# Kernel optimization log

Measured on AMD Instinct MI355X. Metric: run time of the kernel, lower is better.

## Reference

```python
import jax, jax.numpy as jnp
import numpy as np

WIN = 32      # window_size
SHIFT = 16    # shift_size
EPS = 1e-5

def layernorm(x, w, b):
    mu = jnp.mean(x, axis=-1, keepdims=True)
    var = jnp.mean(jnp.square(x - mu), axis=-1, keepdims=True)
    return (x - mu) * jax.lax.rsqrt(var + EPS) * w + b

def setup_inputs() -> dict:
    key = jax.random.key(0)
    ks = jax.random.split(key, 6)
    B, N, C, H = 8, 4096, 512, 2048
    nW = N // WIN
    return {
        "q": jax.random.normal(ks[0], (B, N, C), jnp.float32),
        "kv": jax.random.normal(ks[1], (B, N, C), jnp.float32),
        "attn_mask": jax.random.normal(ks[2], (nW, WIN, WIN), jnp.float32),
        "norm1_w": jnp.ones((C,), jnp.float32),
        "norm1_b": jnp.zeros((C,), jnp.float32),
        "norm2_w": jnp.ones((C,), jnp.float32),
        "norm2_b": jnp.zeros((C,), jnp.float32),
        "fc1_w": jax.random.normal(ks[3], (H, C), jnp.float32) * 0.02,
        "fc1_b": jnp.zeros((H,), jnp.float32),
        "fc2_w": jax.random.normal(ks[4], (C, H), jnp.float32) * 0.02,
        "fc2_b": jnp.zeros((C,), jnp.float32),
    }

def reference(q, kv, attn_mask, norm1_w, norm1_b, norm2_w, norm2_b,
              fc1_w, fc1_b, fc2_w, fc2_b):
    B, N, C = q.shape
    nW = N // WIN
    shortcut = kv
    qn = layernorm(q, norm1_w, norm1_b)
    kn = layernorm(kv, norm1_w, norm1_b)
    # cyclic shift
    qs = jnp.roll(qn, -SHIFT, axis=1)
    ks = jnp.roll(kn, -SHIFT, axis=1)
    qw = qs.reshape(B * nW, WIN, C)
    kw = ks.reshape(B * nW, WIN, C)
    attn = jnp.einsum('bic,bjc->bij', qw, kw)
    attn = attn.reshape(B, nW, WIN, WIN) + attn_mask[None]
    attn = jax.nn.softmax(attn.reshape(B * nW, WIN, WIN), axis=-1)
    x = jnp.einsum('bij,bjc->bic', attn, kw)
    x = jnp.swapaxes(x, 1, 2).reshape(B * nW, WIN, C)
    # window reverse + reverse shift
    x = x.reshape(B, N, C)
    x = jnp.roll(x, SHIFT, axis=1)
    kv_out = shortcut + x
    # MLP (exact erf GELU, dropout identity at eval)
    h = layernorm(kv_out, norm2_w, norm2_b)
    h = jax.nn.gelu(h @ fc1_w.T + fc1_b, approximate=False)
    h = h @ fc2_w.T + fc2_b
    return kv_out + h
```

## Files before the change

### kernel.cpp

```cpp
#include <hip/hip_runtime.h>
#include <cstdint>
#include <cstddef>


typedef __attribute__((ext_vector_type(4)))  float f32x4;
typedef __attribute__((ext_vector_type(16))) float f32x16;
typedef __attribute__((ext_vector_type(8)))  __bf16 bf16x8;
typedef __attribute__((ext_vector_type(8)))  unsigned short us8;
typedef __attribute__((ext_vector_type(4)))  unsigned short us4;

__device__ __forceinline__ unsigned short f2bf(float f) {
  unsigned int u = __builtin_bit_cast(unsigned int, f);
  u += 0x7fffu + ((u >> 16) & 1u);
  return (unsigned short)(u >> 16);
}

#define GLDS16(g, l)                                                         \
  __builtin_amdgcn_global_load_lds(                                          \
      (const __attribute__((address_space(1))) void*)(g),                    \
      (__attribute__((address_space(3))) void*)(l), 16, 0, 0)

__global__ __launch_bounds__(256) void wconv_kernel(
    const float* __restrict__ w1, const float* __restrict__ w2,
    unsigned short* __restrict__ o1, unsigned short* __restrict__ o2) {
  const int i = (blockIdx.x * 256 + threadIdx.x) * 4;
  const f32x4 a = *(const f32x4*)(w1 + i);
  us4 pa; pa[0]=f2bf(a[0]); pa[1]=f2bf(a[1]); pa[2]=f2bf(a[2]); pa[3]=f2bf(a[3]);
  *(us4*)(o1 + i) = pa;
  const f32x4 b = *(const f32x4*)(w2 + i);
  us4 pb; pb[0]=f2bf(b[0]); pb[1]=f2bf(b[1]); pb[2]=f2bf(b[2]); pb[3]=f2bf(b[3]);
  *(us4*)(o2 + i) = pb;
}

__global__ __launch_bounds__(256) void stats_kernel(
    const float* __restrict__ qg, const float* __restrict__ kvg,
    float* __restrict__ stats) {
  const int gw = (blockIdx.x * 256 + threadIdx.x) >> 6;
  const int l  = threadIdx.x & 63;
  const int s  = gw & 1;
  const int row = gw >> 1;
  const float* src = (s ? kvg : qg) + (size_t)row * 512 + l * 8;
  const f32x4 v0 = *(const f32x4*)(src);
  const f32x4 v1 = *(const f32x4*)(src + 4);
  float a = 0.f, a2 = 0.f;
#pragma unroll
  for (int m = 0; m < 4; ++m) {
    a += v0[m] + v1[m];
    a2 += v0[m] * v0[m] + v1[m] * v1[m];
  }
#pragma unroll
  for (int mm = 1; mm <= 32; mm <<= 1) {
    a += __shfl_xor(a, mm); a2 += __shfl_xor(a2, mm);
  }
  if (l == 0) {
    const float mu = a * (1.f / 512.f);
    const float rs = rsqrtf(a2 * (1.f / 512.f) - mu * mu + 1e-5f);
    *(float2*)(stats + (size_t)row * 4 + s * 2) = make_float2(mu, rs);
  }
}

__global__ __launch_bounds__(128) void attn2_kernel(
    const float* __restrict__ qg, const float* __restrict__ kvg,
    const float* __restrict__ maskg,
    const float* __restrict__ n1w, const float* __restrict__ n1b,
    const float* __restrict__ n2w, const float* __restrict__ n2b,
    const float* __restrict__ stats,
    float* __restrict__ kv_out, unsigned short* __restrict__ hn) {
  __shared__ __align__(16) float xch[2][4][64][4];

  const int t  = threadIdx.x;
  const int h  = t >> 6;
  const int l  = t & 63;
  const int il = l & 31;
  const int hi = l >> 5;
  const int g  = blockIdx.x;
  const int b  = g >> 7;
  const int wi = g & 127;
  const int wbase = wi * 32 + 16;

  const int nrow = (wbase + il) & 4095;
  const size_t rowidx = (size_t)b * 4096 + nrow;
  const float* qrow = qg  + rowidx * 512;
  const float* krow = kvg + rowidx * 512;
  const f32x4 st = *(const f32x4*)(stats + rowidx * 4);

  f32x16 sacc = {};
#pragma unroll
  for (int t16 = 0; t16 < 16; ++t16) {
    const int kk = h * 256 + t16 * 16 + hi * 8;
    const f32x4 qa = *(const f32x4*)(qrow + kk);
    const f32x4 qb = *(const f32x4*)(qrow + kk + 4);
    const f32x4 ka = *(const f32x4*)(krow + kk);
    const f32x4 kb = *(const f32x4*)(krow + kk + 4);
    const f32x4 wa = *(const f32x4*)(n1w + kk);
    const f32x4 wb = *(const f32x4*)(n1w + kk + 4);
    const f32x4 ba = *(const f32x4*)(n1b + kk);
    const f32x4 bb = *(const f32x4*)(n1b + kk + 4);
    bf16x8 qh, ql, kh, kl;
#pragma unroll
    for (int e = 0; e < 8; ++e) {
      const float qe = (e < 4) ? qa[e] : qb[e - 4];
      const float ke = (e < 4) ? ka[e] : kb[e - 4];
      const float we = (e < 4) ? wa[e] : wb[e - 4];
      const float be = (e < 4) ? ba[e] : bb[e - 4];
      const float qn = (qe - st[0]) * st[1] * we + be;
      const float kn = (ke - st[2]) * st[3] * we + be;
      const __bf16 qhb = (__bf16)qn;
      const __bf16 khb = (__bf16)kn;
      qh[e] = qhb; ql[e] = (__bf16)(qn - (float)qhb);
      kh[e] = khb; kl[e] = (__bf16)(kn - (float)khb);
    }
    sacc = __builtin_amdgcn_mfma_f32_32x32x16_bf16(kh, qh, sacc, 0, 0, 0);
    sacc = __builtin_amdgcn_mfma_f32_32x32x16_bf16(kh, ql, sacc, 0, 0, 0);
    sacc = __builtin_amdgcn_mfma_f32_32x32x16_bf16(kl, qh, sacc, 0, 0, 0);
  }

#pragma unroll
  for (int qd = 0; qd < 4; ++qd) {
    f32x4 v = {sacc[qd*4+0], sacc[qd*4+1], sacc[qd*4+2], sacc[qd*4+3]};
    *(f32x4*)&xch[h][qd][l][0] = v;
  }
  __syncthreads();
  float sv[16];
#pragma unroll
  for (int qd = 0; qd < 4; ++qd) {
    const f32x4 v = *(const f32x4*)&xch[1 - h][qd][l][0];
#pragma unroll
    for (int m = 0; m < 4; ++m) sv[qd*4+m] = sacc[qd*4+m] + v[m];
  }

  const float* mrow = maskg + (size_t)wi * 1024 + il * 32;
  float mx = -1e30f;
#pragma unroll
  for (int r = 0; r < 16; ++r) {
    const int j = (r & 3) + 8 * (r >> 2) + 4 * hi;
    sv[r] += mrow[j];
    mx = fmaxf(mx, sv[r]);
  }
  mx = fmaxf(mx, __shfl_xor(mx, 32));
  float P[16], sum = 0.f;
#pragma unroll
  for (int r = 0; r < 16; ++r) { P[r] = __expf(sv[r] - mx); sum += P[r]; }
  sum += __shfl_xor(sum, 32);
  const float inv = 1.f / sum;

  const float rs_own = st[3];
  const float ms_own = st[2] * st[3];
  float Pp[16], beta = 0.f;
#pragma unroll
  for (int r = 0; r < 16; ++r) {
    const int j = (r & 3) + 8 * (r >> 2) + 4 * hi;
    const float rsj = __shfl(rs_own, j);
    const float msj = __shfl(ms_own, j);
    P[r] *= inv;
    beta -= P[r] * msj;
    Pp[r] = P[r] * rsj;
  }
  beta += __shfl_xor(beta, 32);
  float breg[16];
#pragma unroll
  for (int r = 0; r < 16; ++r) {
    const int ir = (r & 3) + 8 * (r >> 2) + 4 * hi;
    breg[r] = __shfl(beta, ir);
  }

  float Ps[16];
#pragma unroll
  for (int r = 0; r < 16; ++r) Ps[r] = __shfl_xor(Pp[r], 32);
  bf16x8 pa[2];
#pragma unroll
  for (int s = 0; s < 2; ++s) {
#pragma unroll
    for (int m = 0; m < 8; ++m) {
      float v;
      if (m < 4) v = (hi == 0) ? Pp[8*s+m] : Ps[8*s+m+4];
      else       v = (hi == 1) ? Pp[8*s+m] : Ps[8*s+m-4];
      pa[s][m] = (__bf16)v;
    }
  }

  const size_t bbase = (size_t)b * 4096;
#pragma unroll 2
  for (int nt = 0; nt < 8; ++nt) {
    const int c = h * 256 + nt * 32 + il;
    const float* kvc = kvg + bbase * 512 + c;
    bf16x8 pb0, pb1;
#pragma unroll
    for (int e = 0; e < 8; ++e) {
      const int j0 = 8 * hi + e;
      const int r0 = (wbase + j0) & 4095;
      pb0[e] = (__bf16)kvc[(size_t)r0 * 512];
      const int r1 = (wbase + j0 + 16) & 4095;
      pb1[e] = (__bf16)kvc[(size_t)r1 * 512];
    }
    f32x16 x = {};
    x = __builtin_amdgcn_mfma_f32_32x32x16_bf16(pa[0], pb0, x, 0, 0, 0);
    x = __builtin_amdgcn_mfma_f32_32x32x16_bf16(pa[1], pb1, x, 0, 0, 0);

    const int p  = h * 16 + nt * 2 + (il >> 4);
    const int np = (wbase + p) & 4095;
    const size_t orow = (bbase + np) * 512;
    const float w1c = n1w[c], b1c = n1b[c];
    float ov[16], s1 = 0.f, s2 = 0.f;
#pragma unroll
    for (int qd = 0; qd < 4; ++qd) {
      const int q0 = (il & 15) * 32 + 8 * qd + 4 * hi;
      const f32x4 rv = *(const f32x4*)(kvg + orow + q0);
      f32x4 o;
#pragma unroll
      for (int m = 0; m < 4; ++m) {
        const int r = qd * 4 + m;
        const float xv = w1c * (x[r] + breg[r]) + b1c;
        o[m] = xv + rv[m];
        s1 += o[m]; s2 += o[m] * o[m];
        ov[r] = o[m];
      }
      *(f32x4*)(kv_out + orow + q0) = o;
    }
#pragma unroll
    for (int mm = 1; mm <= 8; mm <<= 1) {
      s1 += __shfl_xor(s1, mm); s2 += __shfl_xor(s2, mm);
    }
    s1 += __shfl_xor(s1, 32); s2 += __shfl_xor(s2, 32);
    const float mu2 = s1 * (1.f / 512.f);
    const float rr  = rsqrtf(s2 * (1.f / 512.f) - mu2 * mu2 + 1e-5f);
#pragma unroll
    for (int qd = 0; qd < 4; ++qd) {
      const int q0 = (il & 15) * 32 + 8 * qd + 4 * hi;
      const f32x4 w2v = *(const f32x4*)(n2w + q0);
      const f32x4 b2v = *(const f32x4*)(n2b + q0);
      us4 hh;
#pragma unroll
      for (int m = 0; m < 4; ++m)
        hh[m] = f2bf((ov[qd*4+m] - mu2) * rr * w2v[m] + b2v[m]);
      *(us4*)(hn + orow + q0) = hh;
    }
  }
}

__global__ __launch_bounds__(256) void gemm1_kernel(
    const unsigned short* __restrict__ A, const unsigned short* __restrict__ Bw,
    const float* __restrict__ bias, unsigned short* __restrict__ Y) {
  __shared__ __align__(16) char smem[32768];

  const int tid = threadIdx.x;
  const int m0 = blockIdx.x << 7;
  const int n0 = blockIdx.y << 7;
  const int l  = tid & 63;
  const int wv = tid >> 6;
  const int wr = wv >> 1, wc = wv & 1;
  const int srow = tid >> 2;
  const int scol = (tid & 3) << 3;
  const int lrow = l & 15;
  const int lko  = (l >> 4) << 3;

  f32x4 acc[4][4] = {};
  const unsigned short* pA = A  + (size_t)(m0 + srow) * 512 + scol;
  const unsigned short* pB = Bw + (size_t)(n0 + srow) * 512 + scol;

#define G1_STAGE(p, kt)                                                      \
  {                                                                          \
    char* base = smem + (p) * 16384;                                         \
    GLDS16(pA + (kt) * 32,            base + wv * 1024);                     \
    GLDS16(pA + 64 * 512 + (kt) * 32, base + 4096 + wv * 1024);              \
    GLDS16(pB + (kt) * 32,            base + 8192 + wv * 1024);              \
    GLDS16(pB + 64 * 512 + (kt) * 32, base + 12288 + wv * 1024);             \
  }

  G1_STAGE(0, 0);
  __syncthreads();
  for (int kt = 0; kt < 16; ++kt) {
    const int p = kt & 1;
    if (kt < 15) G1_STAGE(p ^ 1, kt + 1);
    const unsigned short* As = (const unsigned short*)(smem + p * 16384);
    const unsigned short* Bs = As + 4096;
    bf16x8 af[4], bfr[4];
#pragma unroll
    for (int mi = 0; mi < 4; ++mi)
      af[mi] = *(const bf16x8*)(As + (wr * 64 + mi * 16 + lrow) * 32 + lko);
#pragma unroll
    for (int ni = 0; ni < 4; ++ni)
      bfr[ni] = *(const bf16x8*)(Bs + (wc * 64 + ni * 16 + lrow) * 32 + lko);
#pragma unroll
    for (int mi = 0; mi < 4; ++mi)
#pragma unroll
      for (int ni = 0; ni < 4; ++ni)
        acc[mi][ni] = __builtin_amdgcn_mfma_f32_16x16x32_bf16(
            af[mi], bfr[ni], acc[mi][ni], 0, 0, 0);
    __syncthreads();
  }

  float bn[4];
#pragma unroll
  for (int ni = 0; ni < 4; ++ni) bn[ni] = bias[n0 + wc * 64 + ni * 16 + (l & 15)];

  unsigned short* Ct = (unsigned short*)(smem + wv * 8192);
#pragma unroll
  for (int mi = 0; mi < 4; ++mi)
#pragma unroll
    for (int ni = 0; ni < 4; ++ni)
#pragma unroll
      for (int r = 0; r < 4; ++r) {
        float v = acc[mi][ni][r] + bn[ni];
        v = 0.5f * v * (1.f + erff(v * 0.70710678118654752f));
        const int row  = mi * 16 + ((l >> 4) << 2) + r;
        const int colb = (((ni * 16 + (l & 15)) << 1)) ^ ((row & 7) << 4);
        *(unsigned short*)((char*)Ct + row * 128 + colb) = f2bf(v);
      }
  __syncthreads();
#pragma unroll
  for (int it = 0; it < 8; ++it) {
    const int row = it * 8 + (l >> 3);
    const int off = ((l & 7) << 4) ^ ((row & 7) << 4);
    const us8 v = *(const us8*)((char*)Ct + row * 128 + off);
    const int grow = m0 + wr * 64 + row;
    const int gcol = n0 + wc * 64 + ((l & 7) << 3);
    *(us8*)(Y + (size_t)grow * 2048 + gcol) = v;
  }
}

__global__ __launch_bounds__(256) void gemm2_kernel(
    const unsigned short* __restrict__ A, const unsigned short* __restrict__ Bw,
    const float* __restrict__ bias, const float* __restrict__ res,
    float* __restrict__ out) {
  __shared__ __align__(16) char smem[32768];

  const int tid = threadIdx.x;
  const int m0 = blockIdx.x << 7;
  const int n0 = blockIdx.y << 7;
  const int l  = tid & 63;
  const int wv = tid >> 6;
  const int wr = wv >> 1, wc = wv & 1;
  const int srow = tid >> 2;
  const int scol = (tid & 3) << 3;
  const int lrow = l & 15;
  const int lko  = (l >> 4) << 3;

  f32x4 acc[4][4] = {};
  const unsigned short* pA = A  + (size_t)(m0 + srow) * 2048 + scol;
  const unsigned short* pB = Bw + (size_t)(n0 + srow) * 2048 + scol;

#define G2_STAGE(p, kt)                                                      \
  {                                                                          \
    char* base = smem + (p) * 16384;                                         \
    GLDS16(pA + (kt) * 32,             base + wv * 1024);                    \
    GLDS16(pA + 64 * 2048 + (kt) * 32, base + 4096 + wv * 1024);             \
    GLDS16(pB + (kt) * 32,             base + 8192 + wv * 1024);             \
    GLDS16(pB + 64 * 2048 + (kt) * 32, base + 12288 + wv * 1024);            \
  }

  G2_STAGE(0, 0);
  __syncthreads();
  for (int kt = 0; kt < 64; ++kt) {
    const int p = kt & 1;
    if (kt < 63) G2_STAGE(p ^ 1, kt + 1);
    const unsigned short* As = (const unsigned short*)(smem + p * 16384);
    const unsigned short* Bs = As + 4096;
    bf16x8 af[4], bfr[4];
#pragma unroll
    for (int mi = 0; mi < 4; ++mi)
      af[mi] = *(const bf16x8*)(As + (wr * 64 + mi * 16 + lrow) * 32 + lko);
#pragma unroll
    for (int ni = 0; ni < 4; ++ni)
      bfr[ni] = *(const bf16x8*)(Bs + (wc * 64 + ni * 16 + lrow) * 32 + lko);
#pragma unroll
    for (int mi = 0; mi < 4; ++mi)
#pragma unroll
      for (int ni = 0; ni < 4; ++ni)
        acc[mi][ni] = __builtin_amdgcn_mfma_f32_16x16x32_bf16(
            af[mi], bfr[ni], acc[mi][ni], 0, 0, 0);
    __syncthreads();
  }

#pragma unroll
  for (int ni = 0; ni < 4; ++ni) {
    const int col = n0 + wc * 64 + ni * 16 + (l & 15);
    const float bb = bias[col];
#pragma unroll
    for (int mi = 0; mi < 4; ++mi)
#pragma unroll
      for (int r = 0; r < 4; ++r) {
        const int row = m0 + wr * 64 + mi * 16 + ((l >> 4) << 2) + r;
        const size_t idx = (size_t)row * 512 + col;
        out[idx] = acc[mi][ni][r] + bb + res[idx];
      }
  }
}

extern "C" void kernel_launch(void* const* d_in, const int* in_sizes, int n_in,
                              void* d_out, int out_size, void* d_ws,
                              size_t ws_size, hipStream_t stream) {
  const float* q   = (const float*)d_in[0];
  const float* kv  = (const float*)d_in[1];
  const float* msk = (const float*)d_in[2];
  const float* n1w = (const float*)d_in[3];
  const float* n1b = (const float*)d_in[4];
  const float* n2w = (const float*)d_in[5];
  const float* n2b = (const float*)d_in[6];
  const float* w1  = (const float*)d_in[7];
  const float* b1  = (const float*)d_in[8];
  const float* w2  = (const float*)d_in[9];
  const float* b2  = (const float*)d_in[10];
  float* out = (float*)d_out;

  char* ws = (char*)d_ws;
  float*          kv_out = (float*)ws;
  unsigned short* hn     = (unsigned short*)(ws + 67108864);
  unsigned short* Y1     = (unsigned short*)(ws + 100663296);
  unsigned short* w1b    = (unsigned short*)(ws + 234881024);
  unsigned short* w2b    = (unsigned short*)(ws + 236978176);
  float*          stats  = (float*)(ws + 239075328);

  hipLaunchKernelGGL(wconv_kernel, dim3(1024), dim3(256), 0, stream,
                     w1, w2, w1b, w2b);
  hipLaunchKernelGGL(stats_kernel, dim3(16384), dim3(256), 0, stream,
                     q, kv, stats);
  hipLaunchKernelGGL(attn2_kernel, dim3(1024), dim3(128), 0, stream,
                     q, kv, msk, n1w, n1b, n2w, n2b, stats, kv_out, hn);
  hipLaunchKernelGGL(gemm1_kernel, dim3(256, 16), dim3(256), 0, stream,
                     hn, w1b, b1, Y1);
  hipLaunchKernelGGL(gemm2_kernel, dim3(256, 4), dim3(256), 0, stream,
                     Y1, w2b, b2, kv_out, out);
}
```

Baseline: 509.6 us.

## Rewrite MLP GEMMs with 256x256 tiles, 4-stage LDS pipeline and swizzled layout

Both MLP GEMMs move from 128x128 tiles with a double buffer to 256x256 tiles with 512 threads, a 4-deep global_load_lds pipeline controlled by explicit vmcnt waits, and XOR-swizzled LDS layouts. Block indices are remapped so neighbouring blocks share tiles in L2, and s_setprio is raised around the MFMA bursts. The goal is higher arithmetic intensity and better overlap of loads with MFMAs. The cost is 128KB of LDS per block, heavy register use for 128 accumulators, and gemm2 launching only 256 blocks, which may underfill the GPU.

```diff
diff --git a/kernel.cpp b/kernel.cpp
--- a/kernel.cpp
+++ b/kernel.cpp
@@ -19,6 +19,15 @@
   __builtin_amdgcn_global_load_lds(                                          \
       (const __attribute__((address_space(1))) void*)(g),                    \
       (__attribute__((address_space(3))) void*)(l), 16, 0, 0)
+
+#define BAR()                                                                \
+  do {                                                                       \
+    asm volatile("" ::: "memory");                                           \
+    __builtin_amdgcn_s_barrier();                                            \
+    asm volatile("" ::: "memory");                                           \
+  } while (0)
+
+#define VMW(n) asm volatile("s_waitcnt vmcnt(" #n ")" ::: "memory")
 
 __global__ __launch_bounds__(256) void wconv_kernel(
     const float* __restrict__ w1, const float* __restrict__ w2,
@@ -238,149 +247,152 @@
   }
 }
 
-__global__ __launch_bounds__(256) void gemm1_kernel(
+#define G_ST(K, slot, kt, chunk, pa, pb)                                      \
+  do {                                                                        \
+    GLDS16((pa) + (size_t)(kt) * 32, smem + (slot) * 16384 + (chunk) * 1024); \
+    GLDS16((pb) + (size_t)(kt) * 32,                                          \
+           smem + 65536 + (slot) * 16384 + (chunk) * 1024);                   \
+  } while (0)
+
+#define G_ITER(K, kt, DOSTAGE, VMTAIL)                                        \
+  {                                                                           \
+    const int slot_ = (kt) & 3;                                               \
+    const int ss_ = ((kt) + 3) & 3;                                           \
+    if (DOSTAGE) G_ST(K, ss_, (kt) + 3, wv, pA0, pB0);                        \
+    const char* Ab = smem + slot_ * 16384 + wm * 8192 + laneoff;              \
+    const char* Bb = smem + 65536 + slot_ * 16384 + wn * 4096 + laneoff;      \
+    bf16x8 bf[4], af[4];                                                      \
+    _Pragma("unroll") for (int ni = 0; ni < 4; ++ni)                          \
+        bf[ni] = *(const bf16x8*)(Bb + ni * 1024);                            \
+    _Pragma("unroll") for (int mi = 0; mi < 4; ++mi)                          \
+        af[mi] = *(const bf16x8*)(Ab + mi * 1024);                            \
+    __builtin_amdgcn_s_setprio(1);                                            \
+    _Pragma("unroll") for (int mi = 0; mi < 4; ++mi)                          \
+        _Pragma("unroll") for (int ni = 0; ni < 4; ++ni)                      \
+            acc[mi][ni] = __builtin_amdgcn_mfma_f32_16x16x32_bf16(            \
+                af[mi], bf[ni], acc[mi][ni], 0, 0, 0);                        \
+    __builtin_amdgcn_s_setprio(0);                                            \
+    BAR();                                                                    \
+    if (DOSTAGE) G_ST(K, ss_, (kt) + 3, wv + 8, pA1, pB1);                    \
+    _Pragma("unroll") for (int mi = 0; mi < 4; ++mi)                          \
+        af[mi] = *(const bf16x8*)(Ab + 4096 + mi * 1024);                     \
+    __builtin_amdgcn_s_setprio(1);                                            \
+    _Pragma("unroll") for (int mi = 0; mi < 4; ++mi)                          \
+        _Pragma("unroll") for (int ni = 0; ni < 4; ++ni)                      \
+            acc[mi + 4][ni] = __builtin_amdgcn_mfma_f32_16x16x32_bf16(        \
+                af[mi], bf[ni], acc[mi + 4][ni], 0, 0, 0);                    \
+    __builtin_amdgcn_s_setprio(0);                                            \
+    VMTAIL;                                                                   \
+    BAR();                                                                    \
+  }
+
+__global__ __launch_bounds__(512, 2) void gemm1_kernel(
     const unsigned short* __restrict__ A, const unsigned short* __restrict__ Bw,
     const float* __restrict__ bias, unsigned short* __restrict__ Y) {
-  __shared__ __align__(16) char smem[32768];
-
+  __shared__ __align__(16) char smem[131072];
   const int tid = threadIdx.x;
-  const int m0 = blockIdx.x << 7;
-  const int n0 = blockIdx.y << 7;
-  const int l  = tid & 63;
-  const int wv = tid >> 6;
-  const int wr = wv >> 1, wc = wv & 1;
-  const int srow = tid >> 2;
-  const int scol = (tid & 3) << 3;
-  const int lrow = l & 15;
-  const int lko  = (l >> 4) << 3;
-
-  f32x4 acc[4][4] = {};
-  const unsigned short* pA = A  + (size_t)(m0 + srow) * 512 + scol;
-  const unsigned short* pB = Bw + (size_t)(n0 + srow) * 512 + scol;
-
-#define G1_STAGE(p, kt)                                                      \
-  {                                                                          \
-    char* base = smem + (p) * 16384;                                         \
-    GLDS16(pA + (kt) * 32,            base + wv * 1024);                     \
-    GLDS16(pA + 64 * 512 + (kt) * 32, base + 4096 + wv * 1024);              \
-    GLDS16(pB + (kt) * 32,            base + 8192 + wv * 1024);              \
-    GLDS16(pB + 64 * 512 + (kt) * 32, base + 12288 + wv * 1024);             \
-  }
-
-  G1_STAGE(0, 0);
-  __syncthreads();
-  for (int kt = 0; kt < 16; ++kt) {
-    const int p = kt & 1;
-    if (kt < 15) G1_STAGE(p ^ 1, kt + 1);
-    const unsigned short* As = (const unsigned short*)(smem + p * 16384);
-    const unsigned short* Bs = As + 4096;
-    bf16x8 af[4], bfr[4];
-#pragma unroll
-    for (int mi = 0; mi < 4; ++mi)
-      af[mi] = *(const bf16x8*)(As + (wr * 64 + mi * 16 + lrow) * 32 + lko);
-#pragma unroll
-    for (int ni = 0; ni < 4; ++ni)
-      bfr[ni] = *(const bf16x8*)(Bs + (wc * 64 + ni * 16 + lrow) * 32 + lko);
-#pragma unroll
-    for (int mi = 0; mi < 4; ++mi)
-#pragma unroll
-      for (int ni = 0; ni < 4; ++ni)
-        acc[mi][ni] = __builtin_amdgcn_mfma_f32_16x16x32_bf16(
-            af[mi], bfr[ni], acc[mi][ni], 0, 0, 0);
-    __syncthreads();
-  }
+  const int l   = tid & 63;
+  const int wv  = tid >> 6;
+  const int wm  = wv >> 2;
+  const int wn  = wv & 3;
+
+  const int bid  = blockIdx.x;
+  const int swz  = (bid & 7) * 128 + (bid >> 3);
+  const int m0   = (swz >> 3) << 8;
+  const int n0   = (swz & 7) << 8;
+
+  const int sw = (((l & 3) ^ ((l >> 3) & 3)) << 3);
+  const unsigned short* pA0 = A  + (size_t)(m0 + wv * 16 + (l >> 2)) * 512 + sw;
+  const unsigned short* pA1 = pA0 + (size_t)128 * 512;
+  const unsigned short* pB0 = Bw + (size_t)(n0 + wv * 16 + (l >> 2)) * 512 + sw;
+  const unsigned short* pB1 = pB0 + (size_t)128 * 512;
+  const int laneoff = ((l & 15) << 6) + (((l >> 4) ^ ((l >> 1) & 3)) << 4);
+
+  f32x4 acc[8][4] = {};
+
+  G_ST(512, 0, 0, wv, pA0, pB0); G_ST(512, 0, 0, wv + 8, pA1, pB1);
+  G_ST(512, 1, 1, wv, pA0, pB0); G_ST(512, 1, 1, wv + 8, pA1, pB1);
+  G_ST(512, 2, 2, wv, pA0, pB0); G_ST(512, 2, 2, wv + 8, pA1, pB1);
+  VMW(8); BAR();
+
+  for (int t = 0; t < 13; ++t) G_ITER(512, t, true, VMW(8));
+  G_ITER(512, 13, false, VMW(4));
+  G_ITER(512, 14, false, VMW(0));
+  G_ITER(512, 15, false, ((void)0));
 
   float bn[4];
 #pragma unroll
-  for (int ni = 0; ni < 4; ++ni) bn[ni] = bias[n0 + wc * 64 + ni * 16 + (l & 15)];
-
-  unsigned short* Ct = (unsigned short*)(smem + wv * 8192);
-#pragma unroll
-  for (int mi = 0; mi < 4; ++mi)
+  for (int ni = 0; ni < 4; ++ni)
+    bn[ni] = bias[n0 + wn * 64 + ni * 16 + (l & 15)];
+  char* Ct = smem + wv * 16384;
+#pragma unroll
+  for (int mi = 0; mi < 8; ++mi)
 #pragma unroll
     for (int ni = 0; ni < 4; ++ni)
 #pragma unroll
       for (int r = 0; r < 4; ++r) {
         float v = acc[mi][ni][r] + bn[ni];
         v = 0.5f * v * (1.f + erff(v * 0.70710678118654752f));
-        const int row  = mi * 16 + ((l >> 4) << 2) + r;
-        const int colb = (((ni * 16 + (l & 15)) << 1)) ^ ((row & 7) << 4);
-        *(unsigned short*)((char*)Ct + row * 128 + colb) = f2bf(v);
+        const int row = mi * 16 + ((l >> 4) << 2) + r;
+        const int cb  = (((ni * 16 + (l & 15)) << 1)) ^ (((row >> 2) & 3) << 5);
+        *(unsigned short*)(Ct + row * 128 + cb) = f2bf(v);
       }
-  __syncthreads();
-#pragma unroll
-  for (int it = 0; it < 8; ++it) {
+  BAR();
+#pragma unroll
+  for (int it = 0; it < 16; ++it) {
     const int row = it * 8 + (l >> 3);
-    const int off = ((l & 7) << 4) ^ ((row & 7) << 4);
-    const us8 v = *(const us8*)((char*)Ct + row * 128 + off);
-    const int grow = m0 + wr * 64 + row;
-    const int gcol = n0 + wc * 64 + ((l & 7) << 3);
+    const int b0  = ((l & 7) << 4) ^ (((row >> 2) & 3) << 5);
+    const us8 v = *(const us8*)(Ct + row * 128 + b0);
+    const int grow = m0 + wm * 128 + row;
+    const int gcol = n0 + wn * 64 + ((l & 7) << 3);
     *(us8*)(Y + (size_t)grow * 2048 + gcol) = v;
   }
 }
 
-__global__ __launch_bounds__(256) void gemm2_kernel(
+__global__ __launch_bounds__(512, 2) void gemm2_kernel(
     const unsigned short* __restrict__ A, const unsigned short* __restrict__ Bw,
     const float* __restrict__ bias, const float* __restrict__ res,
     float* __restrict__ out) {
-  __shared__ __align__(16) char smem[32768];
-
+  __shared__ __align__(16) char smem[131072];
   const int tid = threadIdx.x;
-  const int m0 = blockIdx.x << 7;
-  const int n0 = blockIdx.y << 7;
-  const int l  = tid & 63;
-  const int wv = tid >> 6;
-  const int wr = wv >> 1, wc = wv & 1;
-  const int srow = tid >> 2;
-  const int scol = (tid & 3) << 3;
-  const int lrow = l & 15;
-  const int lko  = (l >> 4) << 3;
-
-  f32x4 acc[4][4] = {};
-  const unsigned short* pA = A  + (size_t)(m0 + srow) * 2048 + scol;
-  const unsigned short* pB = Bw + (size_t)(n0 + srow) * 2048 + scol;
-
-#define G2_STAGE(p, kt)                                                      \
-  {                                                                          \
-    char* base = smem + (p) * 16384;                                         \
-    GLDS16(pA + (kt) * 32,             base + wv * 1024);                    \
-    GLDS16(pA + 64 * 2048 + (kt) * 32, base + 4096 + wv * 1024);             \
-    GLDS16(pB + (kt) * 32,             base + 8192 + wv * 1024);             \
-    GLDS16(pB + 64 * 2048 + (kt) * 32, base + 12288 + wv * 1024);            \
-  }
-
-  G2_STAGE(0, 0);
-  __syncthreads();
-  for (int kt = 0; kt < 64; ++kt) {
-    const int p = kt & 1;
-    if (kt < 63) G2_STAGE(p ^ 1, kt + 1);
-    const unsigned short* As = (const unsigned short*)(smem + p * 16384);
-    const unsigned short* Bs = As + 4096;
-    bf16x8 af[4], bfr[4];
-#pragma unroll
-    for (int mi = 0; mi < 4; ++mi)
-      af[mi] = *(const bf16x8*)(As + (wr * 64 + mi * 16 + lrow) * 32 + lko);
-#pragma unroll
-    for (int ni = 0; ni < 4; ++ni)
-      bfr[ni] = *(const bf16x8*)(Bs + (wc * 64 + ni * 16 + lrow) * 32 + lko);
-#pragma unroll
-    for (int mi = 0; mi < 4; ++mi)
-#pragma unroll
-      for (int ni = 0; ni < 4; ++ni)
-        acc[mi][ni] = __builtin_amdgcn_mfma_f32_16x16x32_bf16(
-            af[mi], bfr[ni], acc[mi][ni], 0, 0, 0);
-    __syncthreads();
-  }
+  const int l   = tid & 63;
+  const int wv  = tid >> 6;
+  const int wm  = wv >> 2;
+  const int wn  = wv & 3;
+
+  const int bid  = blockIdx.x;
+  const int swz  = (bid & 7) * 32 + (bid >> 3);
+  const int m0   = (swz >> 1) << 8;
+  const int n0   = (swz & 1) << 8;
+
+  const int sw = (((l & 3) ^ ((l >> 3) & 3)) << 3);
+  const unsigned short* pA0 = A  + (size_t)(m0 + wv * 16 + (l >> 2)) * 2048 + sw;
+  const unsigned short* pA1 = pA0 + (size_t)128 * 2048;
+  const unsigned short* pB0 = Bw + (size_t)(n0 + wv * 16 + (l >> 2)) * 2048 + sw;
+  const unsigned short* pB1 = pB0 + (size_t)128 * 2048;
+  const int laneoff = ((l & 15) << 6) + (((l >> 4) ^ ((l >> 1) & 3)) << 4);
+
+  f32x4 acc[8][4] = {};
+
+  G_ST(2048, 0, 0, wv, pA0, pB0); G_ST(2048, 0, 0, wv + 8, pA1, pB1);
+  G_ST(2048, 1, 1, wv, pA0, pB0); G_ST(2048, 1, 1, wv + 8, pA1, pB1);
+  G_ST(2048, 2, 2, wv, pA0, pB0); G_ST(2048, 2, 2, wv + 8, pA1, pB1);
+  VMW(8); BAR();
+
+  for (int t = 0; t < 61; ++t) G_ITER(2048, t, true, VMW(8));
+  G_ITER(2048, 61, false, VMW(4));
+  G_ITER(2048, 62, false, VMW(0));
+  G_ITER(2048, 63, false, ((void)0));
 
 #pragma unroll
   for (int ni = 0; ni < 4; ++ni) {
-    const int col = n0 + wc * 64 + ni * 16 + (l & 15);
+    const int col = n0 + wn * 64 + ni * 16 + (l & 15);
     const float bb = bias[col];
 #pragma unroll
-    for (int mi = 0; mi < 4; ++mi)
+    for (int mi = 0; mi < 8; ++mi)
 #pragma unroll
       for (int r = 0; r < 4; ++r) {
-        const int row = m0 + wr * 64 + mi * 16 + ((l >> 4) << 2) + r;
+        const int row = m0 + wm * 128 + mi * 16 + ((l >> 4) << 2) + r;
         const size_t idx = (size_t)row * 512 + col;
         out[idx] = acc[mi][ni][r] + bb + res[idx];
       }
@@ -417,8 +429,8 @@
                      q, kv, stats);
   hipLaunchKernelGGL(attn2_kernel, dim3(1024), dim3(128), 0, stream,
                      q, kv, msk, n1w, n1b, n2w, n2b, stats, kv_out, hn);
-  hipLaunchKernelGGL(gemm1_kernel, dim3(256, 16), dim3(256), 0, stream,
+  hipLaunchKernelGGL(gemm1_kernel, dim3(1024), dim3(512), 0, stream,
                      hn, w1b, b1, Y1);
-  hipLaunchKernelGGL(gemm2_kernel, dim3(256, 4), dim3(256), 0, stream,
+  hipLaunchKernelGGL(gemm2_kernel, dim3(256), dim3(512), 0, stream,
                      Y1, w2b, b2, kv_out, out);
 }
```

Result: faster. 487.3 us (-4.4%).
